# Kernel tuning notes

Measured on AMD Instinct MI355X. Metric: run time of the kernel, lower is better.

The kernel has to match this reference:

```python
import jax, jax.numpy as jnp
import numpy as np
import math

B, T, D = 2, 4096, 2048
H, d_head, C = 16, 128, 64


def binarize(x):
    # sign to {-1,+1} with straight-through estimator (identity gradient)
    s = jnp.where(x >= 0, jnp.ones_like(x), -jnp.ones_like(x))
    return x + jax.lax.stop_gradient(s - x)


def setup_inputs() -> dict:
    key = jax.random.key(0)
    ks = jax.random.split(key, 5)
    w_std = 1.0 / math.sqrt(D)
    return {
        "x": jax.random.normal(ks[0], (B, T, D), dtype=jnp.float32),
        "Wq": jax.random.normal(ks[1], (D, D), dtype=jnp.float32) * w_std,
        "Wk": jax.random.normal(ks[2], (D, D), dtype=jnp.float32) * w_std,
        "Wv": jax.random.normal(ks[3], (D, D), dtype=jnp.float32) * w_std,
        "Wo": jax.random.normal(ks[4], (D, D), dtype=jnp.float32) * w_std,
    }


def reference(x, Wq, Wk, Wv, Wo):
    Bx, Tx, Dx = x.shape
    scale = 1.0 / math.sqrt(d_head)
    # projections (torch Linear: y = x @ W.T), split heads -> [B,H,T,d]
    q = (x @ Wq.T).reshape(Bx, Tx, H, d_head).transpose(0, 2, 1, 3) * scale
    k = binarize((x @ Wk.T).reshape(Bx, Tx, H, d_head).transpose(0, 2, 1, 3))
    v = binarize((x @ Wv.T).reshape(Bx, Tx, H, d_head).transpose(0, 2, 1, 3))
    N = Tx // C  # T chosen divisible by chunk_size
    qc = q.reshape(Bx, H, N, C, d_head)
    kc = k.reshape(Bx, H, N, C, d_head)
    vc = v.reshape(Bx, H, N, C, d_head)
    # intra-chunk causal attention
    mask = jnp.tril(jnp.ones((C, C), dtype=x.dtype))
    intra_scores = jnp.einsum('bhnid,bhnjd->bhnij', qc, kc) * mask
    intra = jnp.einsum('bhnij,bhnjd->bhnid', intra_scores, vc)
    # cross-chunk: exclusive prefix sum of per-chunk k^T v outer products
    chunk_kv = jnp.einsum('bhnci,bhncj->bhnij', kc, vc)  # [B,H,N,d,d]
    cs = jnp.cumsum(chunk_kv, axis=2)
    prefix = cs - chunk_kv  # exclusive cumsum
    cross = jnp.einsum('bhncd,bhnde->bhnce', qc, prefix)
    output = (intra + cross).reshape(Bx, H, Tx, d_head)
    out = output.transpose(0, 2, 1, 3).reshape(Bx, Tx, Dx) @ Wo.T
    final_state = cs[:, :, -1]  # [B,H,d,d]
    return out, final_state
```

## Files before the change

kernel.cpp:

```cpp
#include <hip/hip_runtime.h>
#include <stdint.h>

typedef __attribute__((ext_vector_type(8))) short short8;
typedef __attribute__((ext_vector_type(4))) float f32x4;
typedef unsigned short u16;

__device__ __forceinline__ u16 f2bf(float f) {
  uint32_t u = __builtin_bit_cast(uint32_t, f);
  u = (u + 0x7FFFu + ((u >> 16) & 1u)) >> 16;
  return (u16)u;
}
__device__ __forceinline__ float bf2f(u16 h) {
  uint32_t u = ((uint32_t)h) << 16;
  return __builtin_bit_cast(float, u);
}
__device__ __forceinline__ void lds16(const u16* g, u16* l) {
  __builtin_amdgcn_global_load_lds(
      (const __attribute__((address_space(1))) void*)g,
      (__attribute__((address_space(3))) void*)l, 16, 0, 0);
}
__device__ __forceinline__ int sw256(int i) { return i ^ (((i >> 7) & 7) << 3); }
__device__ __forceinline__ int sw128(int i) { return i ^ (((i >> 6) & 7) << 3); }
__device__ __forceinline__ int swzA64(int i) { return i ^ (((i >> 6) & 7) << 3); }
__device__ __forceinline__ int swzA32(int i) { return i ^ (((i >> 6) & 3) << 3); }

#define SB0() __builtin_amdgcn_sched_barrier(0)
#define BAR() __builtin_amdgcn_s_barrier()
#define VM(n) asm volatile("s_waitcnt vmcnt(" #n ")" ::: "memory")

__global__ __launch_bounds__(256) void split_all(
    const float* __restrict__ x,  const float* __restrict__ Wq,
    const float* __restrict__ Wk, const float* __restrict__ Wv,
    const float* __restrict__ Wo,
    u16* __restrict__ xh, u16* __restrict__ xl,
    u16* __restrict__ qh, u16* __restrict__ kh, u16* __restrict__ kl,
    u16* __restrict__ vh, u16* __restrict__ vl, u16* __restrict__ oh)
{
  const int bid = blockIdx.x, t = threadIdx.x;
  if (bid < 2048) {
    for (int i = bid * 256 + t; i < 2097152; i += 2048 * 256) {
      const float4* s = (const float4*)x + 2 * (size_t)i;
      float4 a = s[0], b = s[1];
      float v[8] = {a.x, a.y, a.z, a.w, b.x, b.y, b.z, b.w};
      short8 hi, lo;
#pragma unroll
      for (int j = 0; j < 8; j++) {
        u16 h = f2bf(v[j]);
        hi[j] = (short)h;
        lo[j] = (short)f2bf(v[j] - bf2f(h));
      }
      ((short8*)xh)[i] = hi;
      ((short8*)xl)[i] = lo;
    }
  } else {
    const int seg = (bid - 2048) >> 9;
    const int sb  = (bid - 2048) & 511;
    const float* W = seg == 0 ? Wq : seg == 1 ? Wk : seg == 2 ? Wv : Wo;
    u16* H = seg == 0 ? qh : seg == 1 ? kh : seg == 2 ? vh : oh;
    u16* L = seg == 1 ? kl : seg == 2 ? vl : nullptr;
    for (int i = sb * 256 + t; i < 524288; i += 512 * 256) {
      const float4* s = (const float4*)W + 2 * (size_t)i;
      float4 a = s[0], b = s[1];
      float v[8] = {a.x, a.y, a.z, a.w, b.x, b.y, b.z, b.w};
      short8 hi, lo;
#pragma unroll
      for (int j = 0; j < 8; j++) {
        u16 h = f2bf(v[j]);
        hi[j] = (short)h;
        lo[j] = (short)f2bf(v[j] - bf2f(h));
      }
      ((short8*)H)[i] = hi;
      if (L) ((short8*)L)[i] = lo;
    }
  }
}

template<int SPLIT, int EPI>
__global__ __launch_bounds__(256, 2) void gemm2b(
    const u16* __restrict__ Ahi, const u16* __restrict__ Alo,
    const u16* __restrict__ Bhi, const u16* __restrict__ Blo,
    u16* __restrict__ outb, float* __restrict__ outf,
    int Mdim, int Ndim, int Kdim)
{
  constexpr int BK   = (SPLIT > 1) ? 32 : 64;
  constexpr int TILE = 128 * BK;
  constexpr int NMAT = (SPLIT > 1) ? 4 : 2;
  constexpr int AOFF_H = 0;
  constexpr int AOFF_L = (SPLIT > 1) ? TILE : 0;
  constexpr int BOFF_H = (SPLIT > 1) ? 2*TILE : TILE;
  constexpr int BOFF_L = (SPLIT > 1) ? 3*TILE : 0;
  __shared__ __align__(16) u16 smem[2 * NMAT * TILE];

  const int t = threadIdx.x, l = t & 63;
  const int w = t >> 6;
  const int wm = w >> 1, wn = w & 1;
  const int fr = l & 15, fs = l >> 4;
  const int sb = (blockIdx.x & 7) * 128 + (blockIdx.x >> 3);
  const int m0 = (sb >> 4) * 128, n0 = (sb & 15) * 128;
  const int NT = Kdim / BK;

  auto STM = [&](const u16* src, int g0, int moff, int nr, int kt, int bufb) {
#pragma unroll
    for (int r = 0; r < nr; r++) {
      int d = r * 2048 + t * 8;
      int row, scol;
      if constexpr (SPLIT == 1) { row = d >> 6; scol = ((d >> 3) & 7) ^ (row & 7); }
      else                      { row = d >> 5; scol = ((d >> 3) & 3) ^ ((row >> 1) & 3); }
      lds16(src + (size_t)(g0 + row) * Kdim + kt * BK + scol * 8,
            smem + bufb + moff + d);
    }
  };
  auto ST_ALL = [&](int kt) {
    if (kt >= NT) return;
    const int bufb = (kt & 1) * NMAT * TILE;
    if constexpr (SPLIT == 1) {
      STM(Ahi, m0, AOFF_H, 4, kt, bufb);
      STM(Bhi, n0, BOFF_H, 4, kt, bufb);
    } else {
      STM(Ahi, m0, AOFF_H, 2, kt, bufb);
      STM(Alo, m0, AOFF_L, 2, kt, bufb);
      STM(Bhi, n0, BOFF_H, 2, kt, bufb);
      STM(Blo, n0, BOFF_L, 2, kt, bufb);
    }
  };

  f32x4 acc[4][4] = {};

  auto RD4 = [&](short8* dst, int bufb, int off, int rowbase) {
#pragma unroll
    for (int f = 0; f < 4; f++) {
      int ia = (rowbase + f*16 + fr)*32 + fs*8;
      dst[f] = *(const short8*)(smem + bufb + off + swzA32(ia));
    }
  };
  auto RD8 = [&](short8* dst, int bufb, int off, int rowbase) {
#pragma unroll
    for (int f = 0; f < 4; f++)
#pragma unroll
      for (int ks = 0; ks < 2; ks++) {
        int ia = (rowbase + f*16 + fr)*64 + ks*32 + fs*8;
        dst[f*2+ks] = *(const short8*)(smem + bufb + off + swzA64(ia));
      }
  };

#define PASS44(RA, RB) do {                                                    \
  __builtin_amdgcn_s_setprio(1);                                               \
  _Pragma("unroll") for (int fm_ = 0; fm_ < 4; fm_++)                          \
    _Pragma("unroll") for (int fn_ = 0; fn_ < 4; fn_++)                        \
      acc[fm_][fn_] = __builtin_amdgcn_mfma_f32_16x16x32_bf16(                 \
          (RA)[fm_], (RB)[fn_], acc[fm_][fn_], 0, 0, 0);                       \
  __builtin_amdgcn_s_setprio(0);                                               \
  SB0();                                                                       \
} while (0)

#define PASS44K(RA, RB) do {                                                   \
  __builtin_amdgcn_s_setprio(1);                                               \
  _Pragma("unroll") for (int fm_ = 0; fm_ < 4; fm_++)                          \
    _Pragma("unroll") for (int fn_ = 0; fn_ < 4; fn_++)                        \
      _Pragma("unroll") for (int ks_ = 0; ks_ < 2; ks_++)                      \
        acc[fm_][fn_] = __builtin_amdgcn_mfma_f32_16x16x32_bf16(               \
            (RA)[fm_*2+ks_], (RB)[fn_*2+ks_], acc[fm_][fn_], 0, 0, 0);         \
  __builtin_amdgcn_s_setprio(0);                                               \
  SB0();                                                                       \
} while (0)

  ST_ALL(0);
  VM(0); BAR();

  if constexpr (SPLIT > 1) {
    for (int T = 0; T < NT; T++) {
      const int cb = (T & 1) * NMAT * TILE;
      short8 Ah[4], Al[4], Bh[4], Bl[4];
      RD4(Ah, cb, AOFF_H, wm*64);
      RD4(Al, cb, AOFF_L, wm*64);
      RD4(Bh, cb, BOFF_H, wn*64);
      RD4(Bl, cb, BOFF_L, wn*64);
      SB0();
      ST_ALL(T + 1);
      SB0();
      PASS44(Ah, Bh);
      PASS44(Ah, Bl);
      PASS44(Al, Bh);
      VM(0); BAR();
    }
  } else {
    for (int T = 0; T < NT; T++) {
      const int cb = (T & 1) * NMAT * TILE;
      short8 A[8], B[8];
      RD8(A, cb, AOFF_H, wm*64);
      RD8(B, cb, BOFF_H, wn*64);
      SB0();
      ST_ALL(T + 1);
      SB0();
      PASS44K(A, B);
      VM(0); BAR();
    }
  }
#undef PASS44
#undef PASS44K

  const float qscale = 0.08838834764831843f;
#pragma unroll
  for (int fm = 0; fm < 4; fm++)
#pragma unroll
    for (int fn = 0; fn < 4; fn++)
#pragma unroll
      for (int r = 0; r < 4; r++) {
        int gm = m0 + wm*64 + fm*16 + fs*4 + r;
        int gn = n0 + wn*64 + fn*16 + fr;
        float val = acc[fm][fn][r];
        if constexpr (EPI == 2) {
          outf[(size_t)gm * Ndim + gn] = val;
        } else {
          int b = gm >> 12, tt = gm & 4095, h = gn >> 7, dd = gn & 127;
          size_t idx = (((size_t)(b*16 + h))*4096 + tt)*128 + dd;
          if constexpr (EPI == 0) outb[idx] = f2bf(val * qscale);
          else                    outb[idx] = (val >= 0.f) ? (u16)0x3F80 : (u16)0xBF80;
        }
      }
}

__global__ void pack_signs(const u16* __restrict__ k, const u16* __restrict__ v,
                           unsigned long long* __restrict__ kp, unsigned long long* __restrict__ vp) {
  const int blk = blockIdx.x;
  const int d = threadIdx.x;
  const int bh = blk >> 6, n = blk & 63;
  size_t base = (((size_t)bh * 4096) + n * 64) * 128 + d;
  unsigned long long kw = 0, vw = 0;
  for (int c = 0; c < 64; c++) {
    kw |= (unsigned long long)(k[base + (size_t)c*128] >> 15) << c;
    vw |= (unsigned long long)(v[base + (size_t)c*128] >> 15) << c;
  }
  kp[(size_t)blk * 128 + d] = kw;
  vp[(size_t)blk * 128 + d] = vw;
}

__global__ __launch_bounds__(256) void scan_kernel(
    const unsigned long long* __restrict__ kp, const unsigned long long* __restrict__ vp,
    short* __restrict__ pfx8, float* __restrict__ fsT)
{
  const int t = threadIdx.x;
  const int bh = blockIdx.x >> 6, ep = blockIdx.x & 63;
  const int e = ep * 2 + (t >> 7), d = t & 127;
  const size_t base = (size_t)bh * 64 * 128;
  int s = 0;
  for (int n = 0; n < 64; n++) {
    if ((n & 7) == 0)
      pfx8[((size_t)(bh*8 + (n>>3))*128 + e)*128 + d] = (short)s;
    unsigned long long kw = kp[base + (size_t)n*128 + d];
    unsigned long long vw = vp[base + (size_t)n*128 + e];
    s += 64 - 2*__popcll(kw ^ vw);
  }
  fsT[((size_t)bh*128 + e)*128 + d] = (float)s;
}

__global__ __launch_bounds__(256) void transpose_fs(const float* __restrict__ fsT,
                                                    float* __restrict__ fstate) {
  __shared__ float tile[32*130];
  const int t = threadIdx.x;
  const int bh = blockIdx.x >> 2, es = (blockIdx.x & 3) * 32;
#pragma unroll
  for (int i = 0; i < 16; i++) {
    int idx = t + i*256;
    int e2 = idx >> 7, d = idx & 127;
    tile[e2*130 + d] = fsT[((size_t)bh*128 + es + e2)*128 + d];
  }
  __syncthreads();
#pragma unroll
  for (int i = 0; i < 16; i++) {
    int idx = t + i*256;
    int d = idx >> 5, e2 = idx & 31;
    fstate[((size_t)bh*128 + d)*128 + es + e2] = tile[e2*130 + d];
  }
}

__global__ __launch_bounds__(256) void fused_attn(
    const u16* __restrict__ q, const u16* __restrict__ k,
    const unsigned long long* __restrict__ kp, const unsigned long long* __restrict__ vp,
    const short* __restrict__ pfx8, u16* __restrict__ att)
{
  __shared__ __align__(16) u16 smem[28672];
  u16* sQ  = smem;
  u16* sP1 = smem + 8192;
  u16* sP2 = smem + 16384;
  u16* sS  = smem + 24576;

  const int t = threadIdx.x, l = t & 63, w = t >> 6;
  const int blk = blockIdx.x, bh = blk >> 6, n = blk & 63;
  const int b = bh >> 4, hh = bh & 15;
  const int fr = l & 15, fs = l >> 4;
  const size_t qbase = (((size_t)bh * 4096) + n * 64) * 128;
  const size_t pbase = (size_t)bh * 64 * 128;

#pragma unroll
  for (int i = 0; i < 4; i++) {
    int arow = i*16 + (t>>4);
    int aslot = (t & 15) ^ (arow & 7);
    size_t g = qbase + (size_t)arow*128 + aslot*8;
    lds16(q + g, sQ + i*2048 + t*8);
    lds16(k + g, sP1 + i*2048 + t*8);
  }
  {
    int d = t >> 1, ch = (t & 1) * 32;
    unsigned long long wv = vp[pbase + (size_t)n*128 + d];
#pragma unroll
    for (int c = 0; c < 32; c += 2) {
      uint32_t b0 = ((wv >> (ch + c)) & 1ull)     ? 0xBF80u : 0x3F80u;
      uint32_t b1 = ((wv >> (ch + c + 1)) & 1ull) ? 0xBF80u : 0x3F80u;
      int li = d*64 + ch + c;
      *(uint32_t*)(sP2 + sw128(li)) = b0 | (b1 << 16);
    }
  }
  __syncthreads();

  f32x4 accS[4] = {};
#pragma unroll
  for (int kk = 0; kk < 4; kk++) {
    int la = (w*16 + fr)*128 + kk*32 + fs*8;
    short8 a = *(const short8*)(sQ + sw256(la));
#pragma unroll
    for (int fn = 0; fn < 4; fn++) {
      int lb = (fn*16 + fr)*128 + kk*32 + fs*8;
      short8 bb = *(const short8*)(sP1 + sw256(lb));
      accS[fn] = __builtin_amdgcn_mfma_f32_16x16x32_bf16(a, bb, accS[fn], 0, 0, 0);
    }
  }
#pragma unroll
  for (int fn = 0; fn < 4; fn++)
#pragma unroll
    for (int r = 0; r < 4; r++) {
      int i = w*16 + fs*4 + r, j = fn*16 + fr;
      float v = (j <= i) ? accS[fn][r] : 0.f;
      sS[sw128(i*64 + j)] = f2bf(v);
    }
  __syncthreads();

  f32x4 accI[8] = {};
#pragma unroll
  for (int kk = 0; kk < 2; kk++) {
    int la = (w*16 + fr)*64 + kk*32 + fs*8;
    short8 a = *(const short8*)(sS + sw128(la));
#pragma unroll
    for (int fn = 0; fn < 8; fn++) {
      int lb = (fn*16 + fr)*64 + kk*32 + fs*8;
      short8 bb = *(const short8*)(sP2 + sw128(lb));
      accI[fn] = __builtin_amdgcn_mfma_f32_16x16x32_bf16(a, bb, accI[fn], 0, 0, 0);
    }
  }
  __syncthreads();

  const int m0 = n & ~7, cnt = n & 7;
  for (int hf = 0; hf < 2; hf++) {
#pragma unroll
    for (int p = 0; p < 4; p++) {
      int erow = p*16 + (t>>4);
      int e = hf*64 + erow;
      const short* ps = pfx8 + ((size_t)(bh*8 + (n>>3))*128 + e)*128 + (t&15)*8;
      short8 pv = *(const short8*)ps;
      int accj[8];
#pragma unroll
      for (int j = 0; j < 8; j++) accj[j] = pv[j];
      for (int m = 0; m < cnt; m++) {
        unsigned long long vw = vp[pbase + (size_t)(m0+m)*128 + e];
#pragma unroll
        for (int j = 0; j < 8; j++) {
          unsigned long long kw = kp[pbase + (size_t)(m0+m)*128 + (t&15)*8 + j];
          accj[j] += 64 - 2*__popcll(kw ^ vw);
        }
      }
      short8 hi, lo;
#pragma unroll
      for (int j = 0; j < 8; j++) {
        hi[j] = (short)f2bf((float)(accj[j] >> 5));
        lo[j] = (short)f2bf((float)(accj[j] & 31));
      }
      int pi = sw256(erow*128 + (t&15)*8);
      *(short8*)(sP1 + pi) = hi;
      *(short8*)(sP2 + pi) = lo;
    }
    __syncthreads();

    f32x4 acch[4] = {}, accl[4] = {};
#pragma unroll
    for (int kk = 0; kk < 4; kk++) {
      int la = (w*16 + fr)*128 + kk*32 + fs*8;
      short8 a = *(const short8*)(sQ + sw256(la));
#pragma unroll
      for (int fn = 0; fn < 4; fn++) {
        int pb = sw256((fn*16 + fr)*128 + kk*32 + fs*8);
        acch[fn] = __builtin_amdgcn_mfma_f32_16x16x32_bf16(a, *(const short8*)(sP1 + pb), acch[fn], 0, 0, 0);
        accl[fn] = __builtin_amdgcn_mfma_f32_16x16x32_bf16(a, *(const short8*)(sP2 + pb), accl[fn], 0, 0, 0);
      }
    }
#pragma unroll
    for (int fn = 0; fn < 4; fn++)
#pragma unroll
      for (int r = 0; r < 4; r++) {
        int c = w*16 + fs*4 + r;
        int dcol = hf*64 + fn*16 + fr;
        float val = accI[hf*4+fn][r] + 32.f*acch[fn][r] + accl[fn][r];
        size_t idx = ((size_t)(b*4096 + n*64 + c))*2048 + hh*128 + dcol;
        att[idx] = f2bf(val);
      }
    __syncthreads();
  }
}

extern "C" void kernel_launch(void* const* d_in, const int* in_sizes, int n_in,
                              void* d_out, int out_size, void* d_ws, size_t ws_size,
                              hipStream_t stream) {
  (void)in_sizes; (void)n_in; (void)out_size; (void)ws_size;
  const float* x  = (const float*)d_in[0];
  const float* Wq = (const float*)d_in[1];
  const float* Wk = (const float*)d_in[2];
  const float* Wv = (const float*)d_in[3];
  const float* Wo = (const float*)d_in[4];
  float* out = (float*)d_out;
  float* fstate = out + (size_t)16777216;

  char* ws = (char*)d_ws;
  u16* x_hi = (u16*)(ws + 0);
  u16* x_lo = (u16*)(ws + 33554432);
  u16* qb   = (u16*)(ws + 67108864);
  u16* kb   = (u16*)(ws + 100663296);
  u16* vb   = (u16*)(ws + 134217728);
  u16* wq_h = (u16*)(ws + 167772160);
  u16* wk_h = (u16*)(ws + 176160768);
  u16* wk_l = (u16*)(ws + 184549376);
  u16* wv_h = (u16*)(ws + 192937984);
  u16* wv_l = (u16*)(ws + 201326592);
  u16* wo_h = (u16*)(ws + 209715200);
  unsigned long long* kpk = (unsigned long long*)(ws + 218103808);
  unsigned long long* vpk = (unsigned long long*)(ws + 220200960);
  u16* att    = x_hi;
  float* fsT  = (float*)(ws + 33554432);
  short* pfx8 = (short*)(ws + 134217728);

  split_all<<<4096, 256, 0, stream>>>(x, Wq, Wk, Wv, Wo,
                                      x_hi, x_lo, wq_h, wk_h, wk_l, wv_h, wv_l, wo_h);

  gemm2b<1,0><<<1024, 256, 0, stream>>>(x_hi, nullptr, wq_h, nullptr, qb, nullptr, 8192, 2048, 2048);
  gemm2b<3,1><<<1024, 256, 0, stream>>>(x_hi, x_lo, wk_h, wk_l, kb, nullptr, 8192, 2048, 2048);
  gemm2b<3,1><<<1024, 256, 0, stream>>>(x_hi, x_lo, wv_h, wv_l, vb, nullptr, 8192, 2048, 2048);

  pack_signs<<<2048, 128, 0, stream>>>(kb, vb, kpk, vpk);
  scan_kernel<<<2048, 256, 0, stream>>>(kpk, vpk, pfx8, fsT);
  transpose_fs<<<128, 256, 0, stream>>>(fsT, fstate);
  fused_attn<<<2048, 256, 0, stream>>>(qb, kb, kpk, vpk, pfx8, att);

  gemm2b<1,2><<<1024, 256, 0, stream>>>(att, nullptr, wo_h, nullptr, nullptr, out, 8192, 2048, 2048);
}
```

Measured before the change: 755.6 us.

## Use 256x256 GEMM tiles with 8 waves and phased load/MFMA interleave

Replaces the 128x128, 4-wave GEMM with a 256x256 tile using 512 threads (8 waves, each computing 128x64). The main loop is split into phases, each issuing global-to-LDS loads for the next K tile between MFMA groups, with barriers and waitcnts placed to overlap memory traffic with compute. The larger tile is meant to raise arithmetic intensity and cut redundant global loads. In exchange it doubles shared memory, raises register pressure from 32 accumulator fragments, adds many barriers per iteration, and launches only 256 blocks, which may leave some of the GPU's compute units underused.

```diff
diff --git a/kernel.cpp b/kernel.cpp
--- a/kernel.cpp
+++ b/kernel.cpp
@@ -26,6 +26,7 @@
 
 #define SB0() __builtin_amdgcn_sched_barrier(0)
 #define BAR() __builtin_amdgcn_s_barrier()
+#define LGKM0() do { asm volatile("s_waitcnt lgkmcnt(0)" ::: "memory"); SB0(); } while (0)
 #define VM(n) asm volatile("s_waitcnt vmcnt(" #n ")" ::: "memory")
 
 __global__ __launch_bounds__(256) void split_all(
@@ -76,14 +77,14 @@
 }
 
 template<int SPLIT, int EPI>
-__global__ __launch_bounds__(256, 2) void gemm2b(
+__global__ __launch_bounds__(512, 2) void gemmph(
     const u16* __restrict__ Ahi, const u16* __restrict__ Alo,
     const u16* __restrict__ Bhi, const u16* __restrict__ Blo,
     u16* __restrict__ outb, float* __restrict__ outf,
     int Mdim, int Ndim, int Kdim)
 {
   constexpr int BK   = (SPLIT > 1) ? 32 : 64;
-  constexpr int TILE = 128 * BK;
+  constexpr int TILE = 256 * BK;
   constexpr int NMAT = (SPLIT > 1) ? 4 : 2;
   constexpr int AOFF_H = 0;
   constexpr int AOFF_L = (SPLIT > 1) ? TILE : 0;
@@ -93,120 +94,127 @@
 
   const int t = threadIdx.x, l = t & 63;
   const int w = t >> 6;
-  const int wm = w >> 1, wn = w & 1;
+  const int wm = w >> 2, wn = w & 3;
   const int fr = l & 15, fs = l >> 4;
-  const int sb = (blockIdx.x & 7) * 128 + (blockIdx.x >> 3);
-  const int m0 = (sb >> 4) * 128, n0 = (sb & 15) * 128;
+  const int sb = (blockIdx.x & 7) * 32 + (blockIdx.x >> 3);
+  const int m0 = (sb >> 3) * 256, n0 = (sb & 7) * 256;
   const int NT = Kdim / BK;
 
-  auto STM = [&](const u16* src, int g0, int moff, int nr, int kt, int bufb) {
-#pragma unroll
-    for (int r = 0; r < nr; r++) {
-      int d = r * 2048 + t * 8;
-      int row, scol;
-      if constexpr (SPLIT == 1) { row = d >> 6; scol = ((d >> 3) & 7) ^ (row & 7); }
-      else                      { row = d >> 5; scol = ((d >> 3) & 3) ^ ((row >> 1) & 3); }
-      lds16(src + (size_t)(g0 + row) * Kdim + kt * BK + scol * 8,
-            smem + bufb + moff + d);
-    }
-  };
-  auto ST_ALL = [&](int kt) {
+  auto ST = [&](const u16* src, int g0, int moff, int kt, int r) {
     if (kt >= NT) return;
     const int bufb = (kt & 1) * NMAT * TILE;
-    if constexpr (SPLIT == 1) {
-      STM(Ahi, m0, AOFF_H, 4, kt, bufb);
-      STM(Bhi, n0, BOFF_H, 4, kt, bufb);
-    } else {
-      STM(Ahi, m0, AOFF_H, 2, kt, bufb);
-      STM(Alo, m0, AOFF_L, 2, kt, bufb);
-      STM(Bhi, n0, BOFF_H, 2, kt, bufb);
-      STM(Blo, n0, BOFF_L, 2, kt, bufb);
-    }
+    int d = r * 4096 + t * 8;
+    int row, scol;
+    if constexpr (SPLIT == 1) { row = d >> 6; scol = ((d >> 3) & 7) ^ (row & 7); }
+    else                      { row = d >> 5; scol = ((d >> 3) & 3) ^ ((row >> 1) & 3); }
+    lds16(src + (size_t)(g0 + row) * Kdim + kt * BK + scol * 8,
+          smem + bufb + moff + d);
   };
 
-  f32x4 acc[4][4] = {};
-
-  auto RD4 = [&](short8* dst, int bufb, int off, int rowbase) {
+  f32x4 acc[8][4] = {};
+
+  auto RDA32 = [&](short8* dst, int bufb, int off, int rh) {
 #pragma unroll
     for (int f = 0; f < 4; f++) {
-      int ia = (rowbase + f*16 + fr)*32 + fs*8;
+      int ia = (wm*128 + (rh*4+f)*16 + fr)*32 + fs*8;
       dst[f] = *(const short8*)(smem + bufb + off + swzA32(ia));
     }
   };
-  auto RD8 = [&](short8* dst, int bufb, int off, int rowbase) {
-#pragma unroll
-    for (int f = 0; f < 4; f++)
-#pragma unroll
-      for (int ks = 0; ks < 2; ks++) {
-        int ia = (rowbase + f*16 + fr)*64 + ks*32 + fs*8;
-        dst[f*2+ks] = *(const short8*)(smem + bufb + off + swzA64(ia));
-      }
+  auto RDB32 = [&](short8* dst, int bufb, int off) {
+#pragma unroll
+    for (int fn = 0; fn < 4; fn++) {
+      int ib = (wn*64 + fn*16 + fr)*32 + fs*8;
+      dst[fn] = *(const short8*)(smem + bufb + off + swzA32(ib));
+    }
   };
-
-#define PASS44(RA, RB) do {                                                    \
+  auto RDA64 = [&](short8* dst, int bufb, int rh, int ks) {
+#pragma unroll
+    for (int f = 0; f < 4; f++) {
+      int ia = (wm*128 + (rh*4+f)*16 + fr)*64 + ks*32 + fs*8;
+      dst[f] = *(const short8*)(smem + bufb + AOFF_H + swzA64(ia));
+    }
+  };
+  auto RDB64 = [&](short8* dst, int bufb, int ks) {
+#pragma unroll
+    for (int fn = 0; fn < 4; fn++) {
+      int ib = (wn*64 + fn*16 + fr)*64 + ks*32 + fs*8;
+      dst[fn] = *(const short8*)(smem + bufb + BOFF_H + swzA64(ib));
+    }
+  };
+
+#define MF16(RH, RA, RB) do {                                                  \
   __builtin_amdgcn_s_setprio(1);                                               \
-  _Pragma("unroll") for (int fm_ = 0; fm_ < 4; fm_++)                          \
+  _Pragma("unroll") for (int f_ = 0; f_ < 4; f_++)                             \
     _Pragma("unroll") for (int fn_ = 0; fn_ < 4; fn_++)                        \
-      acc[fm_][fn_] = __builtin_amdgcn_mfma_f32_16x16x32_bf16(                 \
-          (RA)[fm_], (RB)[fn_], acc[fm_][fn_], 0, 0, 0);                       \
+      acc[(RH)*4+f_][fn_] = __builtin_amdgcn_mfma_f32_16x16x32_bf16(           \
+          (RA)[f_], (RB)[fn_], acc[(RH)*4+f_][fn_], 0, 0, 0);                  \
   __builtin_amdgcn_s_setprio(0);                                               \
   SB0();                                                                       \
 } while (0)
 
-#define PASS44K(RA, RB) do {                                                   \
-  __builtin_amdgcn_s_setprio(1);                                               \
-  _Pragma("unroll") for (int fm_ = 0; fm_ < 4; fm_++)                          \
-    _Pragma("unroll") for (int fn_ = 0; fn_ < 4; fn_++)                        \
-      _Pragma("unroll") for (int ks_ = 0; ks_ < 2; ks_++)                      \
-        acc[fm_][fn_] = __builtin_amdgcn_mfma_f32_16x16x32_bf16(               \
-            (RA)[fm_*2+ks_], (RB)[fn_*2+ks_], acc[fm_][fn_], 0, 0, 0);         \
-  __builtin_amdgcn_s_setprio(0);                                               \
-  SB0();                                                                       \
-} while (0)
-
-  ST_ALL(0);
-  VM(0); BAR();
-
   if constexpr (SPLIT > 1) {
+    ST(Ahi, m0, AOFF_H, 0, 0); ST(Ahi, m0, AOFF_H, 0, 1);
+    ST(Bhi, n0, BOFF_H, 0, 0); ST(Bhi, n0, BOFF_H, 0, 1);
+    ST(Blo, n0, BOFF_L, 0, 0); ST(Blo, n0, BOFF_L, 0, 1);
+    ST(Alo, m0, AOFF_L, 0, 0); ST(Alo, m0, AOFF_L, 0, 1);
+    VM(0); BAR();
     for (int T = 0; T < NT; T++) {
       const int cb = (T & 1) * NMAT * TILE;
-      short8 Ah[4], Al[4], Bh[4], Bl[4];
-      RD4(Ah, cb, AOFF_H, wm*64);
-      RD4(Al, cb, AOFF_L, wm*64);
-      RD4(Bh, cb, BOFF_H, wn*64);
-      RD4(Bl, cb, BOFF_L, wn*64);
-      SB0();
-      ST_ALL(T + 1);
-      SB0();
-      PASS44(Ah, Bh);
-      PASS44(Ah, Bl);
-      PASS44(Al, Bh);
-      VM(0); BAR();
+      short8 Ah0[4], Ah1[4], Bh[4], Bl[4], Al[4];
+      RDA32(Ah0, cb, AOFF_H, 0); RDB32(Bh, cb, BOFF_H); SB0();
+      ST(Ahi, m0, AOFF_H, T+1, 0); ST(Ahi, m0, AOFF_H, T+1, 1);
+      BAR(); LGKM0(); MF16(0, Ah0, Bh); BAR();
+      RDA32(Ah1, cb, AOFF_H, 1); SB0();
+      ST(Bhi, n0, BOFF_H, T+1, 0); ST(Bhi, n0, BOFF_H, T+1, 1);
+      VM(4);
+      BAR(); LGKM0(); MF16(1, Ah1, Bh); BAR();
+      RDB32(Bl, cb, BOFF_L); SB0();
+      ST(Blo, n0, BOFF_L, T+1, 0);
+      BAR(); LGKM0(); MF16(0, Ah0, Bl); BAR();
+      ST(Blo, n0, BOFF_L, T+1, 1);
+      BAR(); MF16(1, Ah1, Bl); BAR();
+      RDA32(Al, cb, AOFF_L, 0); SB0();
+      ST(Alo, m0, AOFF_L, T+1, 0);
+      BAR(); LGKM0(); MF16(0, Al, Bh); BAR();
+      RDA32(Al, cb, AOFF_L, 1); SB0();
+      ST(Alo, m0, AOFF_L, T+1, 1);
+      VM(4);
+      BAR(); LGKM0(); MF16(1, Al, Bh); BAR();
     }
   } else {
+    ST(Ahi, m0, AOFF_H, 0, 0); ST(Ahi, m0, AOFF_H, 0, 1);
+    ST(Ahi, m0, AOFF_H, 0, 2); ST(Ahi, m0, AOFF_H, 0, 3);
+    ST(Bhi, n0, BOFF_H, 0, 0); ST(Bhi, n0, BOFF_H, 0, 1);
+    ST(Bhi, n0, BOFF_H, 0, 2); ST(Bhi, n0, BOFF_H, 0, 3);
+    VM(0); BAR();
     for (int T = 0; T < NT; T++) {
       const int cb = (T & 1) * NMAT * TILE;
-      short8 A[8], B[8];
-      RD8(A, cb, AOFF_H, wm*64);
-      RD8(B, cb, BOFF_H, wn*64);
-      SB0();
-      ST_ALL(T + 1);
-      SB0();
-      PASS44K(A, B);
-      VM(0); BAR();
-    }
-  }
-#undef PASS44
-#undef PASS44K
+      short8 A0[4], A1[4], B[4];
+      RDA64(A0, cb, 0, 0); RDB64(B, cb, 0); SB0();
+      ST(Ahi, m0, AOFF_H, T+1, 0); ST(Ahi, m0, AOFF_H, T+1, 1);
+      ST(Ahi, m0, AOFF_H, T+1, 2); ST(Ahi, m0, AOFF_H, T+1, 3);
+      BAR(); LGKM0(); MF16(0, A0, B); BAR();
+      RDA64(A1, cb, 1, 0); SB0();
+      ST(Bhi, n0, BOFF_H, T+1, 0); ST(Bhi, n0, BOFF_H, T+1, 1);
+      ST(Bhi, n0, BOFF_H, T+1, 2); ST(Bhi, n0, BOFF_H, T+1, 3);
+      BAR(); LGKM0(); MF16(1, A1, B); BAR();
+      RDA64(A0, cb, 0, 1); RDB64(B, cb, 1); SB0();
+      BAR(); LGKM0(); MF16(0, A0, B); BAR();
+      RDA64(A1, cb, 1, 1); SB0();
+      VM(0);
+      BAR(); LGKM0(); MF16(1, A1, B); BAR();
+    }
+  }
+#undef MF16
 
   const float qscale = 0.08838834764831843f;
 #pragma unroll
-  for (int fm = 0; fm < 4; fm++)
+  for (int fm = 0; fm < 8; fm++)
 #pragma unroll
     for (int fn = 0; fn < 4; fn++)
 #pragma unroll
       for (int r = 0; r < 4; r++) {
-        int gm = m0 + wm*64 + fm*16 + fs*4 + r;
+        int gm = m0 + wm*128 + fm*16 + fs*4 + r;
         int gn = n0 + wn*64 + fn*16 + fr;
         float val = acc[fm][fn][r];
         if constexpr (EPI == 2) {
@@ -439,14 +447,14 @@
   split_all<<<4096, 256, 0, stream>>>(x, Wq, Wk, Wv, Wo,
                                       x_hi, x_lo, wq_h, wk_h, wk_l, wv_h, wv_l, wo_h);
 
-  gemm2b<1,0><<<1024, 256, 0, stream>>>(x_hi, nullptr, wq_h, nullptr, qb, nullptr, 8192, 2048, 2048);
-  gemm2b<3,1><<<1024, 256, 0, stream>>>(x_hi, x_lo, wk_h, wk_l, kb, nullptr, 8192, 2048, 2048);
-  gemm2b<3,1><<<1024, 256, 0, stream>>>(x_hi, x_lo, wv_h, wv_l, vb, nullptr, 8192, 2048, 2048);
+  gemmph<1,0><<<256, 512, 0, stream>>>(x_hi, nullptr, wq_h, nullptr, qb, nullptr, 8192, 2048, 2048);
+  gemmph<3,1><<<256, 512, 0, stream>>>(x_hi, x_lo, wk_h, wk_l, kb, nullptr, 8192, 2048, 2048);
+  gemmph<3,1><<<256, 512, 0, stream>>>(x_hi, x_lo, wv_h, wv_l, vb, nullptr, 8192, 2048, 2048);
 
   pack_signs<<<2048, 128, 0, stream>>>(kb, vb, kpk, vpk);
   scan_kernel<<<2048, 256, 0, stream>>>(kpk, vpk, pfx8, fsT);
   transpose_fs<<<128, 256, 0, stream>>>(fsT, fstate);
   fused_attn<<<2048, 256, 0, stream>>>(qb, kb, kpk, vpk, pfx8, att);
 
-  gemm2b<1,2><<<1024, 256, 0, stream>>>(att, nullptr, wo_h, nullptr, nullptr, out, 8192, 2048, 2048);
-}
+  gemmph<1,2><<<256, 512, 0, stream>>>(att, nullptr, wo_h, nullptr, nullptr, out, 8192, 2048, 2048);
+}
```

Result: slower. 878.1 us (+16.2%).
